# Kernel tuning notes

Hardware: AMD Instinct MI355X
Metric: run time of the kernel (lower is better)

Reference implementation:

```python
import jax, jax.numpy as jnp
import numpy as np

LAPLACIAN = jnp.array([[-1., -1., -1.], [-1., 8., -1.], [-1., -1., -1.]], dtype=jnp.float32)


def setup_inputs() -> dict:
    key = jax.random.key(0)
    k1, k2 = jax.random.split(key)
    pred = jax.random.normal(k1, (8, 19, 512, 512), dtype=jnp.float32)
    target = jax.random.randint(k2, (8, 512, 512), 0, 19, dtype=jnp.int32)
    return {"pred": pred, "target": target}


def _boundary(x):
    # x: [B, C, H, W] -> abs(clamp(laplacian(x))) per (batch, class) plane
    B, C, H, W = x.shape
    xr = x.reshape(B * C, 1, H, W)
    kern = LAPLACIAN[None, None, :, :]  # [O=1, I=1, 3, 3]
    y = jax.lax.conv_general_dilated(xr, kern, window_strides=(1, 1), padding="SAME")
    return jnp.clip(jnp.abs(y), 0.0, 1.0).reshape(B, C, H, W)


def reference(pred, target):
    # softmax over class dim
    p = jax.nn.softmax(pred, axis=1)
    B, C, H, W = p.shape
    # one-hot target masks: (target[i] == c).float()
    onehot = (target[:, None, :, :] == jnp.arange(C, dtype=target.dtype)[None, :, None, None]).astype(p.dtype)
    pb = _boundary(p)
    tb = _boundary(onehot)
    # sum over (b,c) of per-plane MSE, / (B*C)  == global mean of squared diff
    return jnp.mean((pb - tb) ** 2)
```

## Files before the change

kernel.cpp:

```cpp
#include <hip/hip_runtime.h>

#define NB 8
#define NC 19
#define NH 512
#define NW 512
#define HWP (NH * NW)

#define TW 32
#define TH 16
#define HB_W 40
#define HB_H 18
#define PLANE (HB_W * HB_H)
#define NQ_W 10
#define NQUAD (HB_H * NQ_W)
#define NPAIR 10
#define NTHREADS 256

typedef _Float16 h2 __attribute__((ext_vector_type(2)));

static __device__ __forceinline__ unsigned int h2_to_u(h2 v) {
    return __builtin_bit_cast(unsigned int, v);
}
static __device__ __forceinline__ h2 u_to_h2(unsigned int u) {
    return __builtin_bit_cast(h2, u);
}

__global__ __launch_bounds__(NTHREADS, 5) void bl_main(
    const float* __restrict__ pred, const int* __restrict__ target,
    float* __restrict__ partial)
{
    __shared__ unsigned int e_lds[NPAIR][PLANE];
    __shared__ int t_lds[PLANE];

    const int tid = threadIdx.x;
    const int n = blockIdx.x;
    const int tI = ((n & 7) << 9) + (n >> 3);
    const int bz = tI >> 9;
    const int rem = tI & 511;
    const int by = rem >> 4;
    const int bx = rem & 15;

    const int h0 = by * TH - 1;
    const int gx0 = bx * TW - 4;
    const float* predb = pred + (size_t)bz * NC * HWP;
    const int* tgtb = target + (size_t)bz * HWP;

    if (tid < NQUAD) {
        const int r = tid / NQ_W;
        const int q = tid - r * NQ_W;
        const int gh = h0 + r;
        const int gq = gx0 + (q << 2);
        const int ghc = min(max(gh, 0), NH - 1);
        const int gqc = min(max(gq, 0), NW - 4);
        const bool rowok = (gh >= 0) && (gh < NH);
        const float* src = predb + (size_t)ghc * NW + gqc;

        float s0 = 0.f, s1 = 0.f, s2 = 0.f, s3 = 0.f;
        unsigned int pkv[NPAIR][4];

        #pragma unroll
        for (int j = 0; j < NPAIR; ++j) {
            const float4 a = *reinterpret_cast<const float4*>(
                src + (size_t)(2 * j) * HWP);
            float ea0 = __expf(a.x), ea1 = __expf(a.y);
            float ea2 = __expf(a.z), ea3 = __expf(a.w);
            float eb0 = 0.f, eb1 = 0.f, eb2 = 0.f, eb3 = 0.f;
            if (2 * j + 1 < NC) {
                const float4 b = *reinterpret_cast<const float4*>(
                    src + (size_t)(2 * j + 1) * HWP);
                eb0 = __expf(b.x); eb1 = __expf(b.y);
                eb2 = __expf(b.z); eb3 = __expf(b.w);
            }
            s0 += ea0 + eb0; s1 += ea1 + eb1;
            s2 += ea2 + eb2; s3 += ea3 + eb3;
            h2 p;
            p[0] = (_Float16)ea0; p[1] = (_Float16)eb0; pkv[j][0] = h2_to_u(p);
            p[0] = (_Float16)ea1; p[1] = (_Float16)eb1; pkv[j][1] = h2_to_u(p);
            p[0] = (_Float16)ea2; p[1] = (_Float16)eb2; pkv[j][2] = h2_to_u(p);
            p[0] = (_Float16)ea3; p[1] = (_Float16)eb3; pkv[j][3] = h2_to_u(p);
        }

        #define NORM_PX(E, SE)                                              \
        {                                                                   \
            const bool ok = rowok && (gq + (E) >= 0) && (gq + (E) < NW);    \
            const float invf = ok ? __builtin_amdgcn_rcpf(SE) : 0.f;        \
            h2 ih2; ih2[0] = (_Float16)invf; ih2[1] = (_Float16)invf;       \
            _Pragma("unroll")                                               \
            for (int j = 0; j < NPAIR; ++j)                                 \
                pkv[j][E] = h2_to_u(u_to_h2(pkv[j][E]) * ih2);              \
        }
        NORM_PX(0, s0) NORM_PX(1, s1) NORM_PX(2, s2) NORM_PX(3, s3)
        #undef NORM_PX

        const int lb = r * HB_W + (q << 2);
        #pragma unroll
        for (int j = 0; j < NPAIR; ++j) {
            *reinterpret_cast<uint4*>(&e_lds[j][lb]) =
                make_uint4(pkv[j][0], pkv[j][1], pkv[j][2], pkv[j][3]);
        }

        const int4 tv = *reinterpret_cast<const int4*>(
            tgtb + (size_t)ghc * NW + gqc);
        int4 tw;
        tw.x = (rowok && (gq + 0 >= 0) && (gq + 0 < NW)) ? tv.x : 31;
        tw.y = (rowok && (gq + 1 >= 0) && (gq + 1 < NW)) ? tv.y : 31;
        tw.z = (rowok && (gq + 2 >= 0) && (gq + 2 < NW)) ? tv.z : 31;
        tw.w = (rowok && (gq + 3 >= 0) && (gq + 3 < NW)) ? tv.w : 31;
        *reinterpret_cast<int4*>(&t_lds[lb]) = tw;
    }
    __syncthreads();

    const int tx = tid & 31;
    const int ty = tid >> 5;
    const int r0 = ty * 2;

    int twv[4][3];
    #pragma unroll
    for (int dr = 0; dr < 4; ++dr)
        #pragma unroll
        for (int dc = 0; dc < 3; ++dc)
            twv[dr][dc] = t_lds[(r0 + dr) * HB_W + tx + 3 + dc];

    float acc = 0.f;
    unsigned int m2[2];
    #pragma unroll
    for (int k = 0; k < 2; ++k) {
        const int tc = twv[k + 1][1];
        unsigned int m = 0u;
        bool alleq = true;
        #pragma unroll
        for (int dr = 0; dr < 3; ++dr)
            #pragma unroll
            for (int dc = 0; dc < 3; ++dc) {
                const int t = twv[k + dr][dc];
                m |= (1u << (t & 31));
                alleq = alleq && (t == tc);
            }
        m &= 0x7FFFFu;
        if (alleq) m &= ~(1u << tc);
        m2[k] = m;
        acc += (float)__popc(m);
    }

    #pragma unroll
    for (int j = 0; j < NPAIR; ++j) {
        const unsigned int* plane = &e_lds[j][0];
        h2 hs[4], mid[2];
        #pragma unroll
        for (int dr = 0; dr < 4; ++dr) {
            const int base = (r0 + dr) * HB_W + tx + 3;
            const h2 a = u_to_h2(plane[base]);
            const h2 b = u_to_h2(plane[base + 1]);
            const h2 c = u_to_h2(plane[base + 2]);
            hs[dr] = a + b + c;
            if (dr == 1) mid[0] = b;
            if (dr == 2) mid[1] = b;
        }
        const h2 nine = (h2)((_Float16)9.0f);
        #pragma unroll
        for (int k = 0; k < 2; ++k) {
            const h2 s9 = hs[k] + hs[k + 1] + hs[k + 2];
            const h2 lap = mid[k] * nine - s9;
            const unsigned int au = h2_to_u(lap) & 0x7FFF7FFFu;
            const h2 ab = u_to_h2(au);
            const _Float16 one = (_Float16)1.0f;
            const _Float16 p0 = ab[0] < one ? ab[0] : one;
            const _Float16 p1 = ab[1] < one ? ab[1] : one;
            const float f0 = (float)p0;
            const float f1 = (float)p1;
            const unsigned int bits = (m2[k] >> (2 * j)) & 3u;
            const float tb0 = (float)(bits & 1u);
            const float tb1 = (float)(bits >> 1);
            acc += f0 * f0 + f1 * f1 - 2.f * (tb0 * f0 + tb1 * f1);
        }
    }

    #pragma unroll
    for (int off = 32; off > 0; off >>= 1)
        acc += __shfl_down(acc, off, 64);

    __shared__ float wsum[NTHREADS / 64];
    if ((tid & 63) == 0) wsum[tid >> 6] = acc;
    __syncthreads();
    if (tid == 0) {
        float s = 0.f;
        #pragma unroll
        for (int i = 0; i < NTHREADS / 64; ++i) s += wsum[i];
        partial[n] = s;
    }
}

__global__ __launch_bounds__(1024) void bl_reduce(
    const float4* __restrict__ partial, float* __restrict__ out)
{
    const float4 v = partial[threadIdx.x];
    float s = v.x + v.y + v.z + v.w;
    #pragma unroll
    for (int off = 32; off > 0; off >>= 1)
        s += __shfl_down(s, off, 64);
    __shared__ float wsum[16];
    if ((threadIdx.x & 63) == 0) wsum[threadIdx.x >> 6] = s;
    __syncthreads();
    if (threadIdx.x == 0) {
        float t = 0.f;
        #pragma unroll
        for (int i = 0; i < 16; ++i) t += wsum[i];
        out[0] = t * (1.0f / ((float)NB * NC * NH * NW));
    }
}

extern "C" void kernel_launch(void* const* d_in, const int* in_sizes, int n_in,
                              void* d_out, int out_size, void* d_ws, size_t ws_size,
                              hipStream_t stream) {
    const float* pred = (const float*)d_in[0];
    const int* target = (const int*)d_in[1];
    float* partial = (float*)d_ws;

    bl_main<<<dim3(4096), NTHREADS, 0, stream>>>(pred, target, partial);
    bl_reduce<<<1, 1024, 0, stream>>>((const float4*)partial, (float*)d_out);
}
```

Baseline: 38.54 us.

## Compute 2x2 output pixels per thread in upper half and use packed fp16 ops

The stencil phase now runs only on the 128 threads with tid>=128. Each computes a 2x2 block of pixels, reusing row sums and target bitmasks across neighbouring columns. The mask logic is simplified to a popcount==1 test, the squared-error accumulation uses fdot2 on packed halves, and the fp16 packing uses cvt_pkrtz. This trims ALU and LDS reads per pixel, but the lower 128 threads now sit idle during the stencil, and the round-toward-zero conversion changes rounding.

New measurement: 37.82 us. About the same (-1.9%).

```diff
diff --git a/kernel.cpp b/kernel.cpp
--- a/kernel.cpp
+++ b/kernel.cpp
@@ -24,6 +24,26 @@
 static __device__ __forceinline__ h2 u_to_h2(unsigned int u) {
     return __builtin_bit_cast(h2, u);
 }
+
+#if __has_builtin(__builtin_amdgcn_cvt_pkrtz)
+static __device__ __forceinline__ h2 cvt_pk2(float a, float b) {
+    return __builtin_bit_cast(h2, __builtin_amdgcn_cvt_pkrtz(a, b));
+}
+#else
+static __device__ __forceinline__ h2 cvt_pk2(float a, float b) {
+    h2 r; r[0] = (_Float16)a; r[1] = (_Float16)b; return r;
+}
+#endif
+
+#if __has_builtin(__builtin_amdgcn_fdot2)
+static __device__ __forceinline__ float fdot2f(h2 a, h2 b, float c) {
+    return __builtin_amdgcn_fdot2(a, b, c, false);
+}
+#else
+static __device__ __forceinline__ float fdot2f(h2 a, h2 b, float c) {
+    return c + (float)a[0] * (float)b[0] + (float)a[1] * (float)b[1];
+}
+#endif
 
 __global__ __launch_bounds__(NTHREADS, 5) void bl_main(
     const float* __restrict__ pred, const int* __restrict__ target,
@@ -73,18 +93,18 @@
             }
             s0 += ea0 + eb0; s1 += ea1 + eb1;
             s2 += ea2 + eb2; s3 += ea3 + eb3;
-            h2 p;
-            p[0] = (_Float16)ea0; p[1] = (_Float16)eb0; pkv[j][0] = h2_to_u(p);
-            p[0] = (_Float16)ea1; p[1] = (_Float16)eb1; pkv[j][1] = h2_to_u(p);
-            p[0] = (_Float16)ea2; p[1] = (_Float16)eb2; pkv[j][2] = h2_to_u(p);
-            p[0] = (_Float16)ea3; p[1] = (_Float16)eb3; pkv[j][3] = h2_to_u(p);
+            pkv[j][0] = h2_to_u(cvt_pk2(ea0, eb0));
+            pkv[j][1] = h2_to_u(cvt_pk2(ea1, eb1));
+            pkv[j][2] = h2_to_u(cvt_pk2(ea2, eb2));
+            pkv[j][3] = h2_to_u(cvt_pk2(ea3, eb3));
         }
 
         #define NORM_PX(E, SE)                                              \
         {                                                                   \
             const bool ok = rowok && (gq + (E) >= 0) && (gq + (E) < NW);    \
             const float invf = ok ? __builtin_amdgcn_rcpf(SE) : 0.f;        \
-            h2 ih2; ih2[0] = (_Float16)invf; ih2[1] = (_Float16)invf;       \
+            const _Float16 ih = (_Float16)invf;                             \
+            h2 ih2; ih2[0] = ih; ih2[1] = ih;                               \
             _Pragma("unroll")                                               \
             for (int j = 0; j < NPAIR; ++j)                                 \
                 pkv[j][E] = h2_to_u(u_to_h2(pkv[j][E]) * ih2);              \
@@ -110,68 +130,89 @@
     }
     __syncthreads();
 
-    const int tx = tid & 31;
-    const int ty = tid >> 5;
-    const int r0 = ty * 2;
-
-    int twv[4][3];
-    #pragma unroll
-    for (int dr = 0; dr < 4; ++dr)
-        #pragma unroll
-        for (int dc = 0; dc < 3; ++dc)
-            twv[dr][dc] = t_lds[(r0 + dr) * HB_W + tx + 3 + dc];
-
     float acc = 0.f;
-    unsigned int m2[2];
-    #pragma unroll
-    for (int k = 0; k < 2; ++k) {
-        const int tc = twv[k + 1][1];
-        unsigned int m = 0u;
-        bool alleq = true;
-        #pragma unroll
-        for (int dr = 0; dr < 3; ++dr)
+    if (tid >= 128) {
+        const int t = tid - 128;
+        const int u = t & 15;
+        const int s = t >> 4;
+        const int r0 = 2 * s;
+        const int cw = 2 * u + 2;
+
+        int w[4][4];
+        #pragma unroll
+        for (int r = 0; r < 4; ++r) {
+            const int base = (r0 + r) * HB_W + cw;
+            const int2 mdl = *reinterpret_cast<const int2*>(&t_lds[base + 2]);
+            w[r][0] = t_lds[base + 1];
+            w[r][1] = mdl.x;
+            w[r][2] = mdl.y;
+            w[r][3] = t_lds[base + 4];
+        }
+
+        unsigned int rm[2][4];
+        #pragma unroll
+        for (int r = 0; r < 4; ++r) {
+            const unsigned b1 = 1u << w[r][0];
+            const unsigned b2 = 1u << w[r][1];
+            const unsigned b3 = 1u << w[r][2];
+            const unsigned b4 = 1u << w[r][3];
+            const unsigned mm = b2 | b3;
+            rm[0][r] = mm | b1;
+            rm[1][r] = mm | b4;
+        }
+        unsigned int mpx[2][2];
+        #pragma unroll
+        for (int jc = 0; jc < 2; ++jc) {
+            const unsigned mid = rm[jc][1] | rm[jc][2];
             #pragma unroll
-            for (int dc = 0; dc < 3; ++dc) {
-                const int t = twv[k + dr][dc];
-                m |= (1u << (t & 31));
-                alleq = alleq && (t == tc);
-            }
-        m &= 0x7FFFFu;
-        if (alleq) m &= ~(1u << tc);
-        m2[k] = m;
-        acc += (float)__popc(m);
-    }
-
-    #pragma unroll
-    for (int j = 0; j < NPAIR; ++j) {
-        const unsigned int* plane = &e_lds[j][0];
-        h2 hs[4], mid[2];
-        #pragma unroll
-        for (int dr = 0; dr < 4; ++dr) {
-            const int base = (r0 + dr) * HB_W + tx + 3;
-            const h2 a = u_to_h2(plane[base]);
-            const h2 b = u_to_h2(plane[base + 1]);
-            const h2 c = u_to_h2(plane[base + 2]);
-            hs[dr] = a + b + c;
-            if (dr == 1) mid[0] = b;
-            if (dr == 2) mid[1] = b;
-        }
-        const h2 nine = (h2)((_Float16)9.0f);
-        #pragma unroll
-        for (int k = 0; k < 2; ++k) {
-            const h2 s9 = hs[k] + hs[k + 1] + hs[k + 2];
-            const h2 lap = mid[k] * nine - s9;
-            const unsigned int au = h2_to_u(lap) & 0x7FFF7FFFu;
-            const h2 ab = u_to_h2(au);
-            const _Float16 one = (_Float16)1.0f;
-            const _Float16 p0 = ab[0] < one ? ab[0] : one;
-            const _Float16 p1 = ab[1] < one ? ab[1] : one;
-            const float f0 = (float)p0;
-            const float f1 = (float)p1;
-            const unsigned int bits = (m2[k] >> (2 * j)) & 3u;
-            const float tb0 = (float)(bits & 1u);
-            const float tb1 = (float)(bits >> 1);
-            acc += f0 * f0 + f1 * f1 - 2.f * (tb0 * f0 + tb1 * f1);
+            for (int k = 0; k < 2; ++k) {
+                unsigned m = mid | rm[jc][k ? 3 : 0];
+                m = (__popc(m) == 1) ? 0u : (m & 0x7FFFFu);
+                mpx[jc][k] = m;
+                acc += (float)__popc(m);
+            }
+        }
+
+        h2 one2;  one2[0] = (_Float16)1.f;  one2[1] = (_Float16)1.f;
+        h2 nine2; nine2[0] = (_Float16)9.f; nine2[1] = (_Float16)9.f;
+
+        #pragma unroll
+        for (int j = 0; j < NPAIR; ++j) {
+            const unsigned int* plane = &e_lds[j][0];
+            h2 rs[2][4];
+            h2 ctr[2][2];
+            #pragma unroll
+            for (int r = 0; r < 4; ++r) {
+                const int base = (r0 + r) * HB_W + cw;
+                const uint2 pm = *reinterpret_cast<const uint2*>(&plane[base + 2]);
+                const h2 v1 = u_to_h2(plane[base + 1]);
+                const h2 v2 = u_to_h2(pm.x);
+                const h2 v3 = u_to_h2(pm.y);
+                const h2 v4 = u_to_h2(plane[base + 4]);
+                const h2 tm = v2 + v3;
+                rs[0][r] = v1 + tm;
+                rs[1][r] = tm + v4;
+                if (r == 1) { ctr[0][0] = v2; ctr[1][0] = v3; }
+                if (r == 2) { ctr[0][1] = v2; ctr[1][1] = v3; }
+            }
+            #pragma unroll
+            for (int jc = 0; jc < 2; ++jc) {
+                const h2 midv = rs[jc][1] + rs[jc][2];
+                #pragma unroll
+                for (int k = 0; k < 2; ++k) {
+                    const h2 S = midv + rs[jc][k ? 3 : 0];
+                    const h2 lap = ctr[jc][k] * nine2 - S;
+                    const h2 ab = u_to_h2(h2_to_u(lap) & 0x7FFF7FFFu);
+                    h2 mn;
+                    mn[0] = ab[0] < one2[0] ? ab[0] : one2[0];
+                    mn[1] = ab[1] < one2[1] ? ab[1] : one2[1];
+                    acc = fdot2f(mn, mn, acc);
+                    const unsigned bits = (mpx[jc][k] >> (2 * j)) & 3u;
+                    const unsigned nt = (bits & 1u ? 0x0000C000u : 0u) |
+                                        (bits & 2u ? 0xC0000000u : 0u);
+                    acc = fdot2f(mn, u_to_h2(nt), acc);
+                }
+            }
         }
     }
 
```
